# Kernel tuning notes

Hardware: AMD Instinct MI355X
Metric: run time of the kernel (lower is better)

The kernel has to match this reference:

```python
import jax, jax.numpy as jnp
import numpy as np

EPS = 1e-5
SEQ = 64

def ln(x, g, b):
    m = jnp.mean(x, axis=-1, keepdims=True)
    v = jnp.var(x, axis=-1, keepdims=True)
    return (x - m) / jnp.sqrt(v + EPS) * g + b

def gelu(x):
    return jax.nn.gelu(x, approximate=False)  # torch nn.GELU default = exact erf

def setup_inputs() -> dict:
    key = jax.random.key(0)
    ks = jax.random.split(key, 24)
    B, D = 512, 128
    DSGU = 4 * D          # 512
    DATTN = DSGU // 2     # 256
    DEXP = 4 * D          # 512 (tiny-attn expanded dim)
    TF = SEQ * D          # 8192
    H = int(1.1 * TF)     # 9011
    w = lambda k, s: jax.random.normal(k, s, dtype=jnp.float32) * 0.02
    return {
        "x": jax.random.normal(ks[0], (B, SEQ, D), dtype=jnp.float32),
        # TinyAttentionBlock
        "qkv_ln_g": jnp.ones((D,), jnp.float32), "qkv_ln_b": jnp.zeros((D,), jnp.float32),
        "qkv_w": w(ks[1], (D, 3 * DEXP)), "qkv_b": jnp.zeros((3 * DEXP,), jnp.float32),
        "attn_proj_w": w(ks[2], (DEXP, DATTN)), "attn_proj_b": jnp.zeros((DATTN,), jnp.float32),
        "attn_ln_g": jnp.ones((DATTN,), jnp.float32), "attn_ln_b": jnp.zeros((DATTN,), jnp.float32),
        "rel_bias": w(ks[3], (2 * SEQ - 1,)),
        "scale": jnp.asarray(1.0 / np.sqrt(D), jnp.float32),
        # SGU proj_in / proj_spatial / proj_out
        "pin_ln_g": jnp.ones((D,), jnp.float32), "pin_ln_b": jnp.zeros((D,), jnp.float32),
        "pin_w": w(ks[4], (D, DSGU)), "pin_b": jnp.zeros((DSGU,), jnp.float32),
        "sp_ln_g": jnp.ones((SEQ,), jnp.float32), "sp_ln_b": jnp.zeros((SEQ,), jnp.float32),
        "sp_w": w(ks[5], (SEQ, SEQ)), "sp_b": jnp.ones((SEQ,), jnp.float32),  # bias init 1.0 per source
        "pout_ln_g": jnp.ones((DATTN,), jnp.float32), "pout_ln_b": jnp.zeros((DATTN,), jnp.float32),
        "pout_w": w(ks[6], (DATTN, D)), "pout_b": jnp.zeros((D,), jnp.float32),
        # ResidualBlock MLP
        "mlp_ln_g": jnp.ones((TF,), jnp.float32), "mlp_ln_b": jnp.zeros((TF,), jnp.float32),
        "mlp_w1": w(ks[7], (TF, H)), "mlp_b1": jnp.zeros((H,), jnp.float32),
        "mlp_w2": w(ks[8], (H, TF)), "mlp_b2": jnp.zeros((TF,), jnp.float32),
    }

def reference(x, qkv_ln_g, qkv_ln_b, qkv_w, qkv_b, attn_proj_w, attn_proj_b,
              attn_ln_g, attn_ln_b, rel_bias, scale,
              pin_ln_g, pin_ln_b, pin_w, pin_b, sp_ln_g, sp_ln_b, sp_w, sp_b,
              pout_ln_g, pout_ln_b, pout_w, pout_b,
              mlp_ln_g, mlp_ln_b, mlp_w1, mlp_b1, mlp_w2, mlp_b2):
    B = x.shape[0]
    # --- TinyAttentionBlock ---
    h = ln(x, qkv_ln_g, qkv_ln_b) @ qkv_w + qkv_b          # [B,64,3*512]
    q, k, v = jnp.split(h, 3, axis=-1)                      # each [B,64,512]
    idx = jnp.arange(SEQ)
    rel = idx[None, :] - idx[:, None] + (SEQ - 1)           # [64,64] in [0,126]
    bias = rel_bias[rel]                                    # [64,64]
    attn = jnp.einsum('bnd,bmd->bnm', q, k) + bias
    attn = jax.nn.softmax(attn, axis=-1) * scale            # post-softmax scale (as in source)
    av = jnp.einsum('bnm,bmd->bnd', attn, v)                # [B,64,512]
    a = ln(av @ attn_proj_w + attn_proj_b, attn_ln_g, attn_ln_b)  # [B,64,256]
    # --- SpatialGatingUnit ---
    h2 = gelu(ln(x, pin_ln_g, pin_ln_b) @ pin_w + pin_b)    # [B,64,512]
    u, vv = jnp.split(h2, 2, axis=-1)                        # [B,64,256] each
    vt = jnp.swapaxes(vv, 1, 2)                              # [B,256,64]
    vt = gelu(ln(vt, sp_ln_g, sp_ln_b) @ sp_w + sp_b)        # spatial proj over seq dim
    vv = jnp.swapaxes(vt, 1, 2)                              # [B,64,256]
    out = u * (vv + a)
    out = ln(out, pout_ln_g, pout_ln_b) @ pout_w + pout_b    # [B,64,128]
    x = x + out
    # --- ResidualBlock MLP on flattened board ---
    xf = x.reshape(B, -1)                                    # [B,8192]
    h3 = gelu(ln(xf, mlp_ln_g, mlp_ln_b) @ mlp_w1 + mlp_b1)  # [B,9011]
    xf = xf + (h3 @ mlp_w2 + mlp_b2)
    return xf.reshape(B, SEQ, -1)
```

## Files before the change

### kernel.cpp

```cpp
#include <hip/hip_runtime.h>
#include <hip/hip_bf16.h>
#include <math.h>

typedef float f32x4 __attribute__((ext_vector_type(4)));
typedef float f32x2 __attribute__((ext_vector_type(2)));
typedef short s16x8 __attribute__((ext_vector_type(8)));
typedef short s16x4 __attribute__((ext_vector_type(4)));
typedef int   i32x4 __attribute__((ext_vector_type(4)));

__device__ __forceinline__ short f2bf(float f) {
  __hip_bfloat16 h = __float2bfloat16(f);
  return __builtin_bit_cast(short, h);
}
__device__ __forceinline__ float bf2f(short s) {
  __hip_bfloat16 h = __builtin_bit_cast(__hip_bfloat16, s);
  return __bfloat162float(h);
}
__device__ __forceinline__ float gelu_f(float x) {
  return 0.5f * x * (1.f + erff(x * 0.70710678118654752440f));
}
__device__ __forceinline__ float waveSum(float v) {
  #pragma unroll
  for (int d = 32; d; d >>= 1) v += __shfl_xor(v, d);
  return v;
}
__device__ __forceinline__ void softBarrier() {
  asm volatile("s_waitcnt lgkmcnt(0)" ::: "memory");
  __builtin_amdgcn_s_barrier();
  asm volatile("" ::: "memory");
}

__global__ __launch_bounds__(256) void prep_w_k(
    const float* __restrict__ qkv_w, const float* __restrict__ attn_pw,
    short* __restrict__ wTg, short* __restrict__ pwTg)
{
  int idx = blockIdx.x * 256 + threadIdx.x;
  if (idx < 24576) {
    int r = idx >> 4;
    int k0 = (idx & 15) * 8;
    s16x8 v;
    #pragma unroll
    for (int m = 0; m < 8; ++m) v[m] = f2bf(qkv_w[(size_t)(k0 + m) * 1536 + r]);
    *reinterpret_cast<s16x8*>(&wTg[r * 128 + k0]) = v;
  } else if (idx < 24576 + 16384) {
    int e = idx - 24576;
    int r = e >> 6;
    int k0 = (e & 63) * 8;
    s16x8 v;
    #pragma unroll
    for (int m = 0; m < 8; ++m) v[m] = f2bf(attn_pw[(size_t)(k0 + m) * 256 + r]);
    *reinterpret_cast<s16x8*>(&pwTg[r * 512 + k0]) = v;
  }
}

__global__ __launch_bounds__(256, 2) void fused_attn_k(
    const float* __restrict__ x,
    const float* __restrict__ qln_g, const float* __restrict__ qln_b,
    const float* __restrict__ pln_g, const float* __restrict__ pln_b,
    const short* __restrict__ wTg, const float* __restrict__ qkv_b,
    const short* __restrict__ pwTg, const float* __restrict__ attn_pb,
    const float* __restrict__ aln_g, const float* __restrict__ aln_b,
    const float* __restrict__ relb, const float* __restrict__ scale_p,
    short* __restrict__ lnp, float* __restrict__ ab)
{
  __shared__ __align__(16) char arena[73216];
  short (*lnq)[136] = reinterpret_cast<short(*)[136]>(arena + 0);
  short (*vlds)[72] = reinterpret_cast<short(*)[72]>(arena + 17408);
  short (*avl)[136] = reinterpret_cast<short(*)[136]>(arena + 17408);
  short (*q64)[72]  = reinterpret_cast<short(*)[72]>(arena + 35840);
  short (*k64)[72]  = reinterpret_cast<short(*)[72]>(arena + 45056);
  short (*p64)[72]  = reinterpret_cast<short(*)[72]>(arena + 54272);
  float* sqb  = reinterpret_cast<float*>(arena + 63488);
  float* rb   = reinterpret_cast<float*>(arena + 69632);
  float* sapb = reinterpret_cast<float*>(arena + 70144);
  float* sag  = reinterpret_cast<float*>(arena + 71168);
  float* sab2 = reinterpret_cast<float*>(arena + 72192);

  const int t = threadIdx.x, lane = t & 63, w = t >> 6;
  const int ln15 = lane & 15, hi = lane >> 4;
  const int b = blockIdx.x;

  if (t < 127) rb[t] = relb[t];
  sapb[t] = attn_pb[t]; sag[t] = aln_g[t]; sab2[t] = aln_b[t];
  #pragma unroll
  for (int i = 0; i < 6; ++i) sqb[i*256 + t] = qkv_b[i*256 + t];

  {
    int c = lane * 2;
    float qg0 = qln_g[c], qg1 = qln_g[c+1], qb0 = qln_b[c], qb1 = qln_b[c+1];
    float pg0 = pln_g[c], pg1 = pln_g[c+1], pb0 = pln_b[c], pb1 = pln_b[c+1];
    for (int i = 0; i < 16; ++i) {
      int r = w * 16 + i;
      f32x2 v = *reinterpret_cast<const f32x2*>(&x[((size_t)b*64 + r)*128 + c]);
      float s = v[0] + v[1], sq = v[0]*v[0] + v[1]*v[1];
      s = waveSum(s); sq = waveSum(sq);
      float m = s * (1.f/128.f);
      float rstd = rsqrtf(sq*(1.f/128.f) - m*m + 1e-5f);
      float a0 = (v[0]-m)*rstd, a1 = (v[1]-m)*rstd;
      unsigned u0 = (unsigned short)f2bf(a0*qg0 + qb0);
      unsigned u1 = (unsigned short)f2bf(a1*qg1 + qb1);
      *reinterpret_cast<unsigned*>(&lnq[r][c]) = u0 | (u1 << 16);
      unsigned p0 = (unsigned short)f2bf(a0*pg0 + pb0);
      unsigned p1 = (unsigned short)f2bf(a1*pg1 + pb1);
      ((unsigned*)lnp)[((size_t)b*64 + r)*64 + lane] = p0 | (p1 << 16);
    }
  }
  __syncthreads();

  auto gemm4g = [&](int coff, f32x4 (&acc)[4]) {
    #pragma unroll
    for (int kk = 0; kk < 4; ++kk) {
      s16x8 af = *reinterpret_cast<const s16x8*>(&lnq[w*16 + ln15][kk*32 + hi*8]);
      #pragma unroll
      for (int fn = 0; fn < 4; ++fn) {
        int col = coff + fn*16 + ln15;
        s16x8 bf = *reinterpret_cast<const s16x8*>(&wTg[(size_t)col*128 + kk*32 + hi*8]);
        acc[fn] = __builtin_amdgcn_mfma_f32_16x16x32_bf16(af, bf, acc[fn], 0, 0, 0);
      }
    }
  };
  auto gemm8g = [&](int coff, f32x4 (&acc)[8]) {
    #pragma unroll
    for (int kk = 0; kk < 4; ++kk) {
      s16x8 af = *reinterpret_cast<const s16x8*>(&lnq[w*16 + ln15][kk*32 + hi*8]);
      #pragma unroll
      for (int fn = 0; fn < 8; ++fn) {
        int col = coff + fn*16 + ln15;
        s16x8 bf = *reinterpret_cast<const s16x8*>(&wTg[(size_t)col*128 + kk*32 + hi*8]);
        acc[fn] = __builtin_amdgcn_mfma_f32_16x16x32_bf16(af, bf, acc[fn], 0, 0, 0);
      }
    }
  };

  f32x4 sacc[4] = {};
  for (int kc = 0; kc < 8; ++kc) {
    __syncthreads();
    f32x4 qa[4] = {};
    gemm4g(kc * 64, qa);
    #pragma unroll
    for (int fn = 0; fn < 4; ++fn) {
      float bias = sqb[kc*64 + fn*16 + ln15];
      #pragma unroll
      for (int j = 0; j < 4; ++j)
        q64[w*16 + hi*4 + j][fn*16 + ln15] = f2bf(qa[fn][j] + bias);
    }
    f32x4 ka[4] = {};
    gemm4g(512 + kc * 64, ka);
    #pragma unroll
    for (int fn = 0; fn < 4; ++fn) {
      float bias = sqb[512 + kc*64 + fn*16 + ln15];
      #pragma unroll
      for (int j = 0; j < 4; ++j)
        k64[w*16 + hi*4 + j][fn*16 + ln15] = f2bf(ka[fn][j] + bias);
    }
    __syncthreads();
    #pragma unroll
    for (int kk = 0; kk < 2; ++kk) {
      s16x8 aq = *reinterpret_cast<const s16x8*>(&q64[16*w + ln15][kk*32 + hi*8]);
      #pragma unroll
      for (int fn = 0; fn < 4; ++fn) {
        s16x8 bk = *reinterpret_cast<const s16x8*>(&k64[fn*16 + ln15][kk*32 + hi*8]);
        sacc[fn] = __builtin_amdgcn_mfma_f32_16x16x32_bf16(aq, bk, sacc[fn], 0, 0, 0);
      }
    }
  }

  {
    float scale = scale_p[0];
    #pragma unroll
    for (int j = 0; j < 4; ++j) {
      int row = 16*w + hi*4 + j;
      float pv[4];
      float mx = -1e30f;
      #pragma unroll
      for (int fn = 0; fn < 4; ++fn) {
        int col = fn*16 + ln15;
        pv[fn] = sacc[fn][j] + rb[col - row + 63];
        mx = fmaxf(mx, pv[fn]);
      }
      #pragma unroll
      for (int d = 1; d < 16; d <<= 1) mx = fmaxf(mx, __shfl_xor(mx, d));
      float sum = 0.f;
      #pragma unroll
      for (int fn = 0; fn < 4; ++fn) { pv[fn] = __expf(pv[fn] - mx); sum += pv[fn]; }
      #pragma unroll
      for (int d = 1; d < 16; d <<= 1) sum += __shfl_xor(sum, d);
      float inv = scale / sum;
      #pragma unroll
      for (int fn = 0; fn < 4; ++fn) p64[row][fn*16 + ln15] = f2bf(pv[fn] * inv);
    }
  }

  f32x4 pracc[16] = {};
  for (int cc = 0; cc < 4; ++cc) {
    __syncthreads();
    f32x4 va[8] = {};
    gemm8g(1024 + cc * 128, va);
    #pragma unroll
    for (int fn = 0; fn < 8; ++fn) {
      float bias = sqb[1024 + cc*128 + fn*16 + ln15];
      s16x4 vv;
      #pragma unroll
      for (int j = 0; j < 4; ++j) vv[j] = f2bf(va[fn][j] + bias);
      *reinterpret_cast<s16x4*>(&vlds[fn*16 + ln15][w*16 + hi*4]) = vv;
    }
    __syncthreads();
    f32x4 pacc[8] = {};
    #pragma unroll
    for (int kk = 0; kk < 2; ++kk) {
      s16x8 ap = *reinterpret_cast<const s16x8*>(&p64[16*w + ln15][kk*32 + hi*8]);
      #pragma unroll
      for (int fn = 0; fn < 8; ++fn) {
        s16x8 bv = *reinterpret_cast<const s16x8*>(&vlds[fn*16 + ln15][kk*32 + hi*8]);
        pacc[fn] = __builtin_amdgcn_mfma_f32_16x16x32_bf16(ap, bv, pacc[fn], 0, 0, 0);
      }
    }
    __syncthreads();
    #pragma unroll
    for (int fn = 0; fn < 8; ++fn)
      #pragma unroll
      for (int j = 0; j < 4; ++j)
        avl[w*16 + hi*4 + j][fn*16 + ln15] = f2bf(pacc[fn][j]);
    __syncthreads();
    #pragma unroll
    for (int kk = 0; kk < 4; ++kk) {
      s16x8 aa = *reinterpret_cast<const s16x8*>(&avl[16*w + ln15][kk*32 + hi*8]);
      #pragma unroll
      for (int fn = 0; fn < 16; ++fn) {
        s16x8 pb = *reinterpret_cast<const s16x8*>(
            &pwTg[(size_t)(fn*16 + ln15)*512 + cc*128 + kk*32 + hi*8]);
        pracc[fn] = __builtin_amdgcn_mfma_f32_16x16x32_bf16(aa, pb, pracc[fn], 0, 0, 0);
      }
    }
  }

  #pragma unroll
  for (int j = 0; j < 4; ++j) {
    int row = 16*w + hi*4 + j;
    float vv[16];
    float s = 0.f, sq = 0.f;
    #pragma unroll
    for (int fn = 0; fn < 16; ++fn) {
      vv[fn] = pracc[fn][j] + sapb[fn*16 + ln15];
      s += vv[fn]; sq += vv[fn]*vv[fn];
    }
    #pragma unroll
    for (int d = 1; d < 16; d <<= 1) { s += __shfl_xor(s, d); sq += __shfl_xor(sq, d); }
    float m = s * (1.f/256.f);
    float rstd = rsqrtf(sq*(1.f/256.f) - m*m + 1e-5f);
    #pragma unroll
    for (int fn = 0; fn < 16; ++fn) {
      int col = fn*16 + ln15;
      ab[((size_t)b*64 + row)*256 + col] = (vv[fn]-m)*rstd*sag[col] + sab2[col];
    }
  }
}

template<int BM, int BN, int WM, int WN, int EPI>
__global__ __launch_bounds__(256) void gemm_k(
    const short* __restrict__ A, const float* __restrict__ Bw,
    const float* __restrict__ bias, const float* __restrict__ res,
    void* __restrict__ O0, void* __restrict__ O1,
    int M, int N, int K, int Nreal, int Kreal)
{
  constexpr int BK = 64;
  __shared__ __align__(16) short As[BM][BK + 8];
  __shared__ __align__(16) short Bs[BN][BK + 8];
  const int t = threadIdx.x;
  const int lane = t & 63;
  const int w = t >> 6;
  const int wm = w / WN, wn = w % WN;
  const int ln15 = lane & 15, hi = lane >> 4;
  const int m0 = blockIdx.y * BM;
  const int n0 = blockIdx.x * BN;

  f32x4 acc[4][4] = {};

  for (int k0 = 0; k0 < K; k0 += BK) {
    #pragma unroll
    for (int i = 0; i < (BM*BK)/(256*8); ++i) {
      int e = (i*256 + t) * 8;
      int r = e / BK, c = e % BK;
      *reinterpret_cast<i32x4*>(&As[r][c]) =
          *reinterpret_cast<const i32x4*>(&A[(size_t)(m0 + r) * K + k0 + c]);
    }
    #pragma unroll
    for (int i = 0; i < (BK*BN)/256; ++i) {
      int idx = i*256 + t;
      int n = idx % BN, k = idx / BN;
      int gk = k0 + k, gn = n0 + n;
      float v = (gk < Kreal && gn < Nreal) ? Bw[(size_t)gk * Nreal + gn] : 0.f;
      Bs[n][k] = f2bf(v);
    }
    __syncthreads();
    #pragma unroll
    for (int kk = 0; kk < BK; kk += 32) {
      s16x8 af[4], bfr[4];
      #pragma unroll
      for (int fm = 0; fm < 4; ++fm)
        af[fm] = *reinterpret_cast<const s16x8*>(&As[wm*64 + fm*16 + ln15][kk + hi*8]);
      #pragma unroll
      for (int fn = 0; fn < 4; ++fn)
        bfr[fn] = *reinterpret_cast<const s16x8*>(&Bs[wn*64 + fn*16 + ln15][kk + hi*8]);
      #pragma unroll
      for (int fm = 0; fm < 4; ++fm)
        #pragma unroll
        for (int fn = 0; fn < 4; ++fn)
          acc[fm][fn] = __builtin_amdgcn_mfma_f32_16x16x32_bf16(
              af[fm], bfr[fn], acc[fm][fn], 0, 0, 0);
    }
    __syncthreads();
  }

  #pragma unroll
  for (int fm = 0; fm < 4; ++fm) {
    #pragma unroll
    for (int fn = 0; fn < 4; ++fn) {
      #pragma unroll
      for (int j = 0; j < 4; ++j) {
        int row = m0 + wm*64 + fm*16 + hi*4 + j;
        int col = n0 + wn*64 + fn*16 + ln15;
        float v = acc[fm][fn][j];
        if constexpr (EPI == 2) {
          v = gelu_f(v + bias[col]);
          if (col < 256) ((float*)O0)[(size_t)row * 256 + col] = v;
          else ((short*)O1)[(size_t)row * 256 + (col - 256)] = f2bf(v);
        } else {
          v += bias[col] + res[(size_t)row * N + col];
          ((float*)O0)[(size_t)row * N + col] = v;
        }
      }
    }
  }
}

__global__ __launch_bounds__(256) void ln8192_k(
    const float* __restrict__ x1,
    const float* __restrict__ g, const float* __restrict__ bb,
    short* __restrict__ lnxp)
{
  __shared__ float red[8];
  int t = threadIdx.x, w = t >> 6, lane = t & 63;
  int b = blockIdx.x;
  const f32x4* xr = reinterpret_cast<const f32x4*>(x1 + (size_t)b * 8192);
  f32x4 vals[8];
  float s = 0.f, sq = 0.f;
  #pragma unroll
  for (int i = 0; i < 8; ++i) {
    f32x4 v = xr[t + i*256];
    vals[i] = v;
    s  += v[0]+v[1]+v[2]+v[3];
    sq += v[0]*v[0]+v[1]*v[1]+v[2]*v[2]+v[3]*v[3];
  }
  s = waveSum(s); sq = waveSum(sq);
  if (lane == 0) { red[w] = s; red[4+w] = sq; }
  __syncthreads();
  s  = red[0]+red[1]+red[2]+red[3];
  sq = red[4]+red[5]+red[6]+red[7];
  float m = s * (1.f/8192.f);
  float rstd = rsqrtf(sq * (1.f/8192.f) - m*m + 1e-5f);
  #pragma unroll
  for (int i = 0; i < 8; ++i) {
    int idx = (t + i*256) * 4;
    f32x4 g4 = reinterpret_cast<const f32x4*>(g)[t + i*256];
    f32x4 b4 = reinterpret_cast<const f32x4*>(bb)[t + i*256];
    s16x4 o;
    #pragma unroll
    for (int k = 0; k < 4; ++k) o[k] = f2bf((vals[i][k]-m)*rstd*g4[k] + b4[k]);
    size_t paddr = ((size_t)(idx >> 6) * 512 + b) * 64 + (idx & 63);
    *reinterpret_cast<s16x4*>(&lnxp[paddr]) = o;
  }
}

__global__ __launch_bounds__(512, 2) void gemm_splitk9(
    const short* __restrict__ Ap, const float* __restrict__ Bw,
    float* __restrict__ part,
    int N, int K, int Kreal, int ldb, int kchunk, int ntiles)
{
  __shared__ __align__(16) short Bs[2][128 * 64];
  const int t = threadIdx.x, lane = t & 63, w = t >> 6;
  const int ln15 = lane & 15, hi = lane >> 4;
  const int nt = blockIdx.x % ntiles, z = blockIdx.x / ntiles;
  const int n0 = nt * 128;
  const int kbeg = z * kchunk;
  const int kend = (kbeg + kchunk < K) ? (kbeg + kchunk) : K;
  const int nsteps = (kend - kbeg) >> 6;

  const int bn = t & 127;
  const int bg0 = (t >> 7) * 2;
  const bool bok = (n0 + bn) < ldb;
  const int bsw = bn & 7;

  float br[16];
  auto loadB = [&](int k0) {
    const float* bp = Bw + (size_t)(k0 + bg0 * 8) * ldb + n0 + bn;
    #pragma unroll
    for (int m = 0; m < 16; ++m) {
      int gk = k0 + bg0 * 8 + m;
      br[m] = (bok && gk < Kreal) ? bp[(size_t)m * ldb] : 0.f;
    }
  };
  auto writeB = [&](int buf) {
    s16x8 v0, v1;
    #pragma unroll
    for (int m = 0; m < 8; ++m) { v0[m] = f2bf(br[m]); v1[m] = f2bf(br[8 + m]); }
    short* dst = &Bs[buf][bn * 64];
    *reinterpret_cast<s16x8*>(dst + ((bg0    ) ^ bsw) * 8) = v0;
    *reinterpret_cast<s16x8*>(dst + ((bg0 + 1) ^ bsw) * 8) = v1;
  };

  f32x4 acc[4][8] = {};

  loadB(kbeg);
  writeB(0);
  if (nsteps > 1) loadB(kbeg + 64);
  softBarrier();

  for (int s = 0; s < nsteps; ++s) {
    const int k0 = kbeg + s * 64;
    const short* atile = Ap + (size_t)(k0 >> 6) * 512 * 64;
    s16x8 af[8];
    #pragma unroll
    for (int kk = 0; kk < 2; ++kk)
      #pragma unroll
      for (int fm = 0; fm < 4; ++fm) {
        int row = w * 64 + fm * 16 + ln15;
        af[kk * 4 + fm] = *reinterpret_cast<const s16x8*>(
            &atile[row * 64 + (kk * 4 + hi) * 8]);
      }
    if (s + 1 < nsteps) writeB((s + 1) & 1);
    if (s + 2 < nsteps) loadB(kbeg + (s + 2) * 64);

    const short* bsrc = &Bs[s & 1][0];
    #pragma unroll
    for (int kk = 0; kk < 2; ++kk) {
      const int g = kk * 4 + hi;
      #pragma unroll
      for (int fn = 0; fn < 8; ++fn) {
        int row = fn * 16 + ln15;
        s16x8 bv = *reinterpret_cast<const s16x8*>(
            &bsrc[row * 64 + ((g ^ (row & 7)) * 8)]);
        #pragma unroll
        for (int fm = 0; fm < 4; ++fm)
          acc[fm][fn] = __builtin_amdgcn_mfma_f32_16x16x32_bf16(
              af[kk * 4 + fm], bv, acc[fm][fn], 0, 0, 0);
      }
    }
    softBarrier();
  }

  #pragma unroll
  for (int fm = 0; fm < 4; ++fm)
    #pragma unroll
    for (int fn = 0; fn < 8; ++fn)
      #pragma unroll
      for (int j = 0; j < 4; ++j) {
        int row = w * 64 + fm * 16 + hi * 4 + j;
        int col = n0 + fn * 16 + ln15;
        part[((size_t)z * 512 + row) * N + col] = acc[fm][fn][j];
      }
}

__global__ __launch_bounds__(256) void reduce_mlp1_k(
    const float* __restrict__ part, const float* __restrict__ bias,
    short* __restrict__ h3p, int N, int Nreal, int M, int ks)
{
  int col4 = (blockIdx.x * 256 + threadIdx.x) * 4;
  int row = blockIdx.y;
  if (col4 >= N) return;
  size_t base = (size_t)row * N + col4;
  size_t stride = (size_t)M * N;
  f32x4 s = *reinterpret_cast<const f32x4*>(part + base);
  for (int k = 1; k < ks; ++k)
    s += *reinterpret_cast<const f32x4*>(part + base + (size_t)k * stride);
  s16x4 o;
  #pragma unroll
  for (int j = 0; j < 4; ++j) {
    int c = col4 + j;
    float v = 0.f;
    if (c < Nreal) v = gelu_f(s[j] + bias[c]);
    o[j] = f2bf(v);
  }
  size_t paddr = ((size_t)(col4 >> 6) * 512 + row) * 64 + (col4 & 63);
  *reinterpret_cast<s16x4*>(&h3p[paddr]) = o;
}

__global__ __launch_bounds__(256) void reduce_mlp2_k(
    const float* __restrict__ part, const float* __restrict__ bias,
    const float* __restrict__ x1, float* __restrict__ out, int N, int M, int ks)
{
  int col4 = (blockIdx.x * 256 + threadIdx.x) * 4;
  int row = blockIdx.y;
  size_t base = (size_t)row * N + col4;
  size_t stride = (size_t)M * N;
  f32x4 s = *reinterpret_cast<const f32x4*>(part + base);
  for (int k = 1; k < ks; ++k)
    s += *reinterpret_cast<const f32x4*>(part + base + (size_t)k * stride);
  f32x4 b4 = *reinterpret_cast<const f32x4*>(bias + col4);
  f32x4 r4 = *reinterpret_cast<const f32x4*>(x1 + base);
  #pragma unroll
  for (int j = 0; j < 4; ++j) s[j] += b4[j] + r4[j];
  *reinterpret_cast<f32x4*>(out + base) = s;
}

__global__ __launch_bounds__(256) void gate_k(
    const float* __restrict__ u, const short* __restrict__ vbf,
    const float* __restrict__ a,
    const float* __restrict__ spg_g, const float* __restrict__ spg_b,
    const float* __restrict__ spw, const float* __restrict__ spb,
    const float* __restrict__ pog, const float* __restrict__ pob,
    short* __restrict__ outn)
{
  __shared__ __align__(16) short nvb[256][72];
  __shared__ __align__(16) short spwT[64][72];
  __shared__ float s_spg[64], s_spbl[64], s_spb[64];
  __shared__ float s_pog[256], s_pob[256];
  int t = threadIdx.x, lane = t & 63, w = t >> 6;
  int ln15 = lane & 15, hi = lane >> 4;
  int b = blockIdx.x;

  if (t < 64) { s_spg[t] = spg_g[t]; s_spbl[t] = spg_b[t]; s_spb[t] = spb[t]; }
  s_pog[t] = pog[t]; s_pob[t] = pob[t];
  #pragma unroll
  for (int i = 0; i < 16; ++i) {
    int idx = i*256 + t;
    int sr = idx >> 6, tc = idx & 63;
    spwT[tc][sr] = f2bf(spw[idx]);
  }

  float vvv[64];
  {
    int c = t;
    float s = 0.f, sq = 0.f;
    #pragma unroll
    for (int si = 0; si < 64; ++si) {
      float f = bf2f(vbf[(size_t)(b*64 + si) * 256 + c]);
      vvv[si] = f; s += f; sq += f*f;
    }
    float m = s * (1.f/64.f);
    float rstd = rsqrtf(sq * (1.f/64.f) - m*m + 1e-5f);
    __syncthreads();
    #pragma unroll
    for (int si = 0; si < 64; ++si)
      nvb[c][si] = f2bf((vvv[si]-m)*rstd*s_spg[si] + s_spbl[si]);
  }
  __syncthreads();

  f32x4 yacc[4][4] = {};
  #pragma unroll
  for (int kk = 0; kk < 64; kk += 32) {
    s16x8 af[4], bfr[4];
    #pragma unroll
    for (int fm = 0; fm < 4; ++fm)
      af[fm] = *reinterpret_cast<const s16x8*>(&nvb[64*w + fm*16 + ln15][kk + hi*8]);
    #pragma unroll
    for (int fn = 0; fn < 4; ++fn)
      bfr[fn] = *reinterpret_cast<const s16x8*>(&spwT[fn*16 + ln15][kk + hi*8]);
    #pragma unroll
    for (int fm = 0; fm < 4; ++fm)
      #pragma unroll
      for (int fn = 0; fn < 4; ++fn)
        yacc[fm][fn] = __builtin_amdgcn_mfma_f32_16x16x32_bf16(
            af[fm], bfr[fn], yacc[fm][fn], 0, 0, 0);
  }
  __syncthreads();

  short (*outl)[264] = reinterpret_cast<short(*)[264]>(&nvb[0][0]);
  #pragma unroll
  for (int fm = 0; fm < 4; ++fm) {
    #pragma unroll
    for (int fn = 0; fn < 4; ++fn) {
      int crow = 64*w + fm*16 + hi*4;
      int tcol = fn*16 + ln15;
      f32x4 u4 = *reinterpret_cast<const f32x4*>(&u[(size_t)(b*64 + tcol)*256 + crow]);
      f32x4 a4 = *reinterpret_cast<const f32x4*>(&a[(size_t)(b*64 + tcol)*256 + crow]);
      #pragma unroll
      for (int j = 0; j < 4; ++j) {
        float g = gelu_f(yacc[fm][fn][j] + s_spb[tcol]);
        float o = u4[j] * (g + a4[j]);
        outl[tcol][crow + j] = f2bf(o);
      }
    }
  }
  __syncthreads();

  #pragma unroll
  for (int ri = 0; ri < 16; ++ri) {
    int trow = w*16 + ri;
    int c = lane * 4;
    s16x4 raw = *reinterpret_cast<const s16x4*>(&outl[trow][c]);
    float f0 = bf2f(raw[0]), f1 = bf2f(raw[1]), f2 = bf2f(raw[2]), f3 = bf2f(raw[3]);
    float s  = f0+f1+f2+f3;
    float sq = f0*f0+f1*f1+f2*f2+f3*f3;
    s = waveSum(s); sq = waveSum(sq);
    float m = s * (1.f/256.f);
    float rstd = rsqrtf(sq * (1.f/256.f) - m*m + 1e-5f);
    s16x4 o;
    o[0] = f2bf((f0-m)*rstd*s_pog[c+0] + s_pob[c+0]);
    o[1] = f2bf((f1-m)*rstd*s_pog[c+1] + s_pob[c+1]);
    o[2] = f2bf((f2-m)*rstd*s_pog[c+2] + s_pob[c+2]);
    o[3] = f2bf((f3-m)*rstd*s_pog[c+3] + s_pob[c+3]);
    *reinterpret_cast<s16x4*>(&outn[(size_t)(b*64 + trow)*256 + c]) = o;
  }
}

extern "C" void kernel_launch(void* const* d_in, const int* in_sizes, int n_in,
                              void* d_out, int out_size, void* d_ws, size_t ws_size,
                              hipStream_t stream)
{
  const float* x          = (const float*)d_in[0];
  const float* qkv_ln_g   = (const float*)d_in[1];
  const float* qkv_ln_b   = (const float*)d_in[2];
  const float* qkv_w      = (const float*)d_in[3];
  const float* qkv_b      = (const float*)d_in[4];
  const float* attn_pw    = (const float*)d_in[5];
  const float* attn_pb    = (const float*)d_in[6];
  const float* attn_ln_g  = (const float*)d_in[7];
  const float* attn_ln_b  = (const float*)d_in[8];
  const float* rel_bias   = (const float*)d_in[9];
  const float* scale      = (const float*)d_in[10];
  const float* pin_ln_g   = (const float*)d_in[11];
  const float* pin_ln_b   = (const float*)d_in[12];
  const float* pin_w      = (const float*)d_in[13];
  const float* pin_b      = (const float*)d_in[14];
  const float* sp_ln_g    = (const float*)d_in[15];
  const float* sp_ln_b    = (const float*)d_in[16];
  const float* sp_w       = (const float*)d_in[17];
  const float* sp_b       = (const float*)d_in[18];
  const float* pout_ln_g  = (const float*)d_in[19];
  const float* pout_ln_b  = (const float*)d_in[20];
  const float* pout_w     = (const float*)d_in[21];
  const float* pout_b     = (const float*)d_in[22];
  const float* mlp_ln_g   = (const float*)d_in[23];
  const float* mlp_ln_b   = (const float*)d_in[24];
  const float* mlp_w1     = (const float*)d_in[25];
  const float* mlp_b1     = (const float*)d_in[26];
  const float* mlp_w2     = (const float*)d_in[27];
  const float* mlp_b2     = (const float*)d_in[28];

  char* ws = (char*)d_ws;
  short* lnp   = (short*)(ws + 0);
  float* x1b   = (float*)(ws + 0);
  float* ab    = (float*)(ws + 16777216);
  float* ub    = (float*)(ws + 50331648);
  short* wTg   = (short*)(ws + 83886080);
  short* pwTg  = (short*)(ws + 84279296);
  short* vbfb  = (short*)(ws + 83886080);
  short* outnb = (short*)(ws + 100663296);
  short* lnxp  = (short*)(ws + 150994944);
  short* h3p   = (short*)(ws + 159383552);
  float* partb = (float*)(ws + 16777216);

  prep_w_k<<<160, 256, 0, stream>>>(qkv_w, attn_pw, wTg, pwTg);
  fused_attn_k<<<512, 256, 0, stream>>>(
      x, qkv_ln_g, qkv_ln_b, pin_ln_g, pin_ln_b, wTg, qkv_b,
      pwTg, attn_pb, attn_ln_g, attn_ln_b, rel_bias, scale, lnp, ab);
  gemm_k<128,128,2,2,2><<<dim3(4,256), 256, 0, stream>>>(
      lnp, pin_w, pin_b, nullptr, ub, vbfb, 32768, 512, 128, 512, 128);
  gate_k<<<512, 256, 0, stream>>>(ub, vbfb, ab, sp_ln_g, sp_ln_b, sp_w, sp_b,
                                  pout_ln_g, pout_ln_b, outnb);
  gemm_k<128,128,2,2,3><<<dim3(1,256), 256, 0, stream>>>(
      outnb, pout_w, pout_b, x, x1b, nullptr, 32768, 128, 256, 128, 256);
  ln8192_k<<<512, 256, 0, stream>>>(x1b, mlp_ln_g, mlp_ln_b, lnxp);

  gemm_splitk9<<<213, 512, 0, stream>>>(
      lnxp, mlp_w1, partb, 9088, 8192, 8192,
      9011, 2752, 71);
  reduce_mlp1_k<<<dim3(9, 512), 256, 0, stream>>>(partb, mlp_b1, h3p, 9088, 9011, 512, 3);

  gemm_splitk9<<<256, 512, 0, stream>>>(
      h3p, mlp_w2, partb, 8192, 9088, 9011,
      8192, 2304, 64);
  reduce_mlp2_k<<<dim3(8, 512), 256, 0, stream>>>(partb, mlp_b2, x1b, (float*)d_out, 8192, 512, 4);
}
```

Before: 649.1 us.

## Pre-pack MLP weights to bf16 slices and use LDS-free split-K GEMM

Replaces the fused fp32-weight split-K GEMMs for both MLP layers with a two-phase scheme. For each of four K slices, a transpose kernel converts the fp32 weights into a tiled bf16 layout, and an LDS-free GEMM then loads A and B fragments directly from global memory into MFMA operands. The goal is to remove strided fp32 weight loads, in-loop conversion and LDS barriers from the GEMM inner loop. In exchange, every call pays an extra write and read of the bf16 weight slice and eight more kernel launches, and the GEMM now has no data reuse through shared memory.

```diff
diff --git a/kernel.cpp b/kernel.cpp
--- a/kernel.cpp
+++ b/kernel.cpp
@@ -23,11 +23,6 @@
   #pragma unroll
   for (int d = 32; d; d >>= 1) v += __shfl_xor(v, d);
   return v;
-}
-__device__ __forceinline__ void softBarrier() {
-  asm volatile("s_waitcnt lgkmcnt(0)" ::: "memory");
-  __builtin_amdgcn_s_barrier();
-  asm volatile("" ::: "memory");
 }
 
 __global__ __launch_bounds__(256) void prep_w_k(
@@ -51,6 +46,78 @@
     for (int m = 0; m < 8; ++m) v[m] = f2bf(attn_pw[(size_t)(k0 + m) * 256 + r]);
     *reinterpret_cast<s16x8*>(&pwTg[r * 512 + k0]) = v;
   }
+}
+
+__global__ __launch_bounds__(256) void prep_slice_k(
+    const float* __restrict__ Bw, short* __restrict__ Bp,
+    int ldb, int Kreal, int kbeg, int ntile64, int Npad)
+{
+  __shared__ float tile[64][65];
+  const int nt = blockIdx.x % ntile64, kt = blockIdx.x / ntile64;
+  const int t = threadIdx.x;
+  #pragma unroll
+  for (int i = 0; i < 16; ++i) {
+    int e = i * 256 + t, r = e >> 6, c = e & 63;
+    int gk = kbeg + kt * 64 + r, gn = nt * 64 + c;
+    tile[r][c] = (gk < Kreal && gn < ldb) ? Bw[(size_t)gk * ldb + gn] : 0.f;
+  }
+  __syncthreads();
+  const int c = t >> 2, q = t & 3;
+  s16x8 v0, v1;
+  #pragma unroll
+  for (int m = 0; m < 8; ++m) {
+    v0[m] = f2bf(tile[q*16 + m][c]);
+    v1[m] = f2bf(tile[q*16 + 8 + m][c]);
+  }
+  short* dst = Bp + ((size_t)kt * Npad + nt * 64 + c) * 64 + q * 16;
+  *reinterpret_cast<s16x8*>(dst) = v0;
+  *reinterpret_cast<s16x8*>(dst + 8) = v1;
+}
+
+__global__ __launch_bounds__(256, 3) void gemm_nolds_k(
+    const short* __restrict__ Ap, const short* __restrict__ Bp,
+    float* __restrict__ part,
+    int Npad, int ktbase, int nsteps, int ntiles, int z)
+{
+  const int t = threadIdx.x, lane = t & 63, w = t >> 6;
+  const int ln15 = lane & 15, hi = lane >> 4;
+  const int W = blockIdx.x * 4 + w;
+  const int nt = W % ntiles, rg = W / ntiles;
+  const int m0 = rg * 64, n0 = nt * 64;
+
+  f32x4 acc[4][4] = {};
+
+  for (int s = 0; s < nsteps; ++s) {
+    const short* at = Ap + ((size_t)(ktbase + s) * 512 + m0) * 64;
+    const short* bt = Bp + ((size_t)s * Npad + n0) * 64;
+    s16x8 af[8], bf[8];
+    #pragma unroll
+    for (int kk = 0; kk < 2; ++kk)
+      #pragma unroll
+      for (int f = 0; f < 4; ++f) {
+        af[kk*4 + f] = *reinterpret_cast<const s16x8*>(
+            &at[(f*16 + ln15) * 64 + (kk*4 + hi) * 8]);
+        bf[kk*4 + f] = *reinterpret_cast<const s16x8*>(
+            &bt[(f*16 + ln15) * 64 + (kk*4 + hi) * 8]);
+      }
+    #pragma unroll
+    for (int kk = 0; kk < 2; ++kk)
+      #pragma unroll
+      for (int fm = 0; fm < 4; ++fm)
+        #pragma unroll
+        for (int fn = 0; fn < 4; ++fn)
+          acc[fm][fn] = __builtin_amdgcn_mfma_f32_16x16x32_bf16(
+              af[kk*4 + fm], bf[kk*4 + fn], acc[fm][fn], 0, 0, 0);
+  }
+
+  #pragma unroll
+  for (int fm = 0; fm < 4; ++fm)
+    #pragma unroll
+    for (int fn = 0; fn < 4; ++fn)
+      #pragma unroll
+      for (int j = 0; j < 4; ++j)
+        part[((size_t)z * 512 + m0 + fm*16 + hi*4 + j) * Npad + n0 + fn*16 + ln15]
+            = acc[fm][fn][j];
 }
 
 __global__ __launch_bounds__(256, 2) void fused_attn_k(
@@ -370,95 +437,6 @@
     size_t paddr = ((size_t)(idx >> 6) * 512 + b) * 64 + (idx & 63);
     *reinterpret_cast<s16x4*>(&lnxp[paddr]) = o;
   }
-}
-
-__global__ __launch_bounds__(512, 2) void gemm_splitk9(
-    const short* __restrict__ Ap, const float* __restrict__ Bw,
-    float* __restrict__ part,
-    int N, int K, int Kreal, int ldb, int kchunk, int ntiles)
-{
-  __shared__ __align__(16) short Bs[2][128 * 64];
-  const int t = threadIdx.x, lane = t & 63, w = t >> 6;
-  const int ln15 = lane & 15, hi = lane >> 4;
-  const int nt = blockIdx.x % ntiles, z = blockIdx.x / ntiles;
-  const int n0 = nt * 128;
-  const int kbeg = z * kchunk;
-  const int kend = (kbeg + kchunk < K) ? (kbeg + kchunk) : K;
-  const int nsteps = (kend - kbeg) >> 6;
-
-  const int bn = t & 127;
-  const int bg0 = (t >> 7) * 2;
-  const bool bok = (n0 + bn) < ldb;
-  const int bsw = bn & 7;
-
-  float br[16];
-  auto loadB = [&](int k0) {
-    const float* bp = Bw + (size_t)(k0 + bg0 * 8) * ldb + n0 + bn;
-    #pragma unroll
-    for (int m = 0; m < 16; ++m) {
-      int gk = k0 + bg0 * 8 + m;
-      br[m] = (bok && gk < Kreal) ? bp[(size_t)m * ldb] : 0.f;
-    }
-  };
-  auto writeB = [&](int buf) {
-    s16x8 v0, v1;
-    #pragma unroll
-    for (int m = 0; m < 8; ++m) { v0[m] = f2bf(br[m]); v1[m] = f2bf(br[8 + m]); }
-    short* dst = &Bs[buf][bn * 64];
-    *reinterpret_cast<s16x8*>(dst + ((bg0    ) ^ bsw) * 8) = v0;
-    *reinterpret_cast<s16x8*>(dst + ((bg0 + 1) ^ bsw) * 8) = v1;
-  };
-
-  f32x4 acc[4][8] = {};
-
-  loadB(kbeg);
-  writeB(0);
-  if (nsteps > 1) loadB(kbeg + 64);
-  softBarrier();
-
-  for (int s = 0; s < nsteps; ++s) {
-    const int k0 = kbeg + s * 64;
-    const short* atile = Ap + (size_t)(k0 >> 6) * 512 * 64;
-    s16x8 af[8];
-    #pragma unroll
-    for (int kk = 0; kk < 2; ++kk)
-      #pragma unroll
-      for (int fm = 0; fm < 4; ++fm) {
-        int row = w * 64 + fm * 16 + ln15;
-        af[kk * 4 + fm] = *reinterpret_cast<const s16x8*>(
-            &atile[row * 64 + (kk * 4 + hi) * 8]);
-      }
-    if (s + 1 < nsteps) writeB((s + 1) & 1);
-    if (s + 2 < nsteps) loadB(kbeg + (s + 2) * 64);
-
-    const short* bsrc = &Bs[s & 1][0];
-    #pragma unroll
-    for (int kk = 0; kk < 2; ++kk) {
-      const int g = kk * 4 + hi;
-      #pragma unroll
-      for (int fn = 0; fn < 8; ++fn) {
-        int row = fn * 16 + ln15;
-        s16x8 bv = *reinterpret_cast<const s16x8*>(
-            &bsrc[row * 64 + ((g ^ (row & 7)) * 8)]);
-        #pragma unroll
-        for (int fm = 0; fm < 4; ++fm)
-          acc[fm][fn] = __builtin_amdgcn_mfma_f32_16x16x32_bf16(
-              af[kk * 4 + fm], bv, acc[fm][fn], 0, 0, 0);
-      }
-    }
-    softBarrier();
-  }
-
-  #pragma unroll
-  for (int fm = 0; fm < 4; ++fm)
-    #pragma unroll
-    for (int fn = 0; fn < 8; ++fn)
-      #pragma unroll
-      for (int j = 0; j < 4; ++j) {
-        int row = w * 64 + fm * 16 + hi * 4 + j;
-        int col = n0 + fn * 16 + ln15;
-        part[((size_t)z * 512 + row) * N + col] = acc[fm][fn][j];
-      }
 }
 
 __global__ __launch_bounds__(256) void reduce_mlp1_k(
@@ -650,6 +628,7 @@
   short* lnxp  = (short*)(ws + 150994944);
   short* h3p   = (short*)(ws + 159383552);
   float* partb = (float*)(ws + 16777216);
+  short* Bpb   = (short*)(ws + 92274688);
 
   prep_w_k<<<160, 256, 0, stream>>>(qkv_w, attn_pw, wTg, pwTg);
   fused_attn_k<<<512, 256, 0, stream>>>(
@@ -663,13 +642,27 @@
       outnb, pout_w, pout_b, x, x1b, nullptr, 32768, 128, 256, 128, 256);
   ln8192_k<<<512, 256, 0, stream>>>(x1b, mlp_ln_g, mlp_ln_b, lnxp);
 
-  gemm_splitk9<<<213, 512, 0, stream>>>(
-      lnxp, mlp_w1, partb, 9088, 8192, 8192,
-      9011, 2752, 71);
-  reduce_mlp1_k<<<dim3(9, 512), 256, 0, stream>>>(partb, mlp_b1, h3p, 9088, 9011, 512, 3);
-
-  gemm_splitk9<<<256, 512, 0, stream>>>(
-      h3p, mlp_w2, partb, 8192, 9088, 9011,
-      8192, 2304, 64);
+  for (int z = 0; z < 4; ++z) {
+    prep_slice_k<<<32 * 142, 256, 0, stream>>>(
+        mlp_w1, Bpb, 9011, 8192, z * 2048,
+        142, 9088);
+    gemm_nolds_k<<<284, 256, 0, stream>>>(
+        lnxp, Bpb, partb, 9088, z * 32, 32,
+        142, z);
+  }
+  reduce_mlp1_k<<<dim3(9, 512), 256, 0, stream>>>(partb, mlp_b1, h3p, 9088, 9011, 512, 4);
+
+  {
+    const int ktb[4] = {0, 36, 72, 108};
+    const int kts[4] = {36, 36, 36, 34};
+    for (int z = 0; z < 4; ++z) {
+      prep_slice_k<<<kts[z] * 128, 256, 0, stream>>>(
+          mlp_w2, Bpb, 8192, 9011, ktb[z] * 64,
+          128, 8192);
+      gemm_nolds_k<<<256, 256, 0, stream>>>(
+          h3p, Bpb, partb, 8192, ktb[z], kts[z],
+          128, z);
+    }
+  }
   reduce_mlp2_k<<<dim3(8, 512), 256, 0, stream>>>(partb, mlp_b2, x1b, (float*)d_out, 8192, 512, 4);
 }
```

New measurement: 1.532 ms. 136% more time.
